# Kernel tuning notes

Measured on AMD Instinct MI355X. Metric: run time of the kernel, lower is better.

The kernel has to match this reference:

```python
import jax, jax.numpy as jnp
import numpy as np

B, S, T = 4096, 2048, 2  # batch of conversations, turns per conversation, num_tags


def setup_inputs() -> dict:
    key = jax.random.key(0)
    k1, k2, k3, k4, k5, k6 = jax.random.split(key, 6)
    emissions = jax.random.normal(k1, (B, S, T), dtype=jnp.float32)
    # learned transition matrices for DistanceCRF branch order:
    # [even2odd, I0, D_consecutive, D_nonconsecutive]
    trans_params = jax.random.normal(k2, (4, T, T), dtype=jnp.float32) * 0.1
    tags = jax.random.randint(k3, (B, S), 0, T)
    who2who = jax.random.randint(k4, (B, S), 0, 2)
    intime = jax.random.randint(k5, (B, S), 0, 3)
    distance = jax.random.randint(k6, (B, S), 0, 4)
    return {"emissions": emissions, "trans_params": trans_params, "tags": tags,
            "who2who": who2who, "intime": intime, "distance": distance}


def _select_trans(trans_params, who2who, intime, distance):
    """Per-step transition matrix selection (DistanceCRF logic).
    Returns [B, S, T, T]."""
    Tn = trans_params.shape[-1]
    # index 0 = zero 'padding' matrix (who2who == -1 case)
    bank = jnp.concatenate([jnp.zeros((1, Tn, Tn), trans_params.dtype), trans_params], axis=0)
    sel = jnp.where(who2who == -1, 0,
          jnp.where(who2who == 1, 1,          # even2odd
          jnp.where(intime == 0, 2,           # I0
          jnp.where(distance == 0, 3, 4))))   # D_consecutive / D_nonconsecutive
    return bank[sel]


def reference(emissions, trans_params, tags, who2who, intime, distance):
    Bn, Sn, Tn = emissions.shape
    trans = _select_trans(trans_params, who2who, intime, distance)  # [B,S,T,T]

    # ---- gold path score ----
    em_gold = jnp.take_along_axis(emissions, tags[..., None], axis=-1)[..., 0].sum(-1)  # [B]
    oh_prev = jax.nn.one_hot(tags[:, :-1], Tn, dtype=emissions.dtype)  # [B,S-1,T]
    oh_cur = jax.nn.one_hot(tags[:, 1:], Tn, dtype=emissions.dtype)
    tr_gold = jnp.einsum('bsij,bsi,bsj->b', trans[:, 1:], oh_prev, oh_cur)  # [B]
    gold_score = em_gold + tr_gold

    # ---- log partition via forward recursion (note: transition added at t=0 too,
    # matching the original implementation) ----
    def step(alpha, xs):
        em_t, tr_t = xs  # [B,T], [B,T,T]
        new_alpha = jax.nn.logsumexp(alpha[:, :, None] + em_t[:, None, :] + tr_t, axis=1)
        return new_alpha, None

    alpha0 = jnp.zeros((Bn, Tn), emissions.dtype)
    xs = (jnp.swapaxes(emissions, 0, 1), jnp.swapaxes(trans, 0, 1))  # [S,B,T], [S,B,T,T]
    alpha, _ = jax.lax.scan(step, alpha0, xs)
    total_score = jax.nn.logsumexp(alpha, axis=-1)  # [B]

    return jnp.stack([gold_score, total_score])  # [2, B]
```

## Files before the change

### kernel.cpp

```cpp
#include <hip/hip_runtime.h>
#include <math.h>

#define Bn 4096
#define Sn 2048
#define BLOCK 1024

__global__ __launch_bounds__(BLOCK) void crf_fused(
    const float* __restrict__ emissions,
    const float* __restrict__ trans_params,
    const int*   __restrict__ tags,
    const int*   __restrict__ who2who,
    const int*   __restrict__ intime,
    const int*   __restrict__ distance,
    float*       __restrict__ out)
{
    const int b    = blockIdx.x;
    const int t    = threadIdx.x;
    const int lane = t & 63;
    const int wave = t >> 6;
    const long base = (long)b * Sn;

    __shared__ __align__(16) float lbank[20];
    __shared__ __align__(16) float ebank[20];
    __shared__ float sred[16][8];

    float4 e  = ((const float4*)(emissions + base * 2))[t];
    int2   tg = ((const int2*)(tags     + base))[t];
    int2   wh = ((const int2*)(who2who  + base))[t];
    int2   it = ((const int2*)(intime   + base))[t];
    int2   ds = ((const int2*)(distance + base))[t];
    int ptag = 0;
    if (lane == 0 && t > 0) ptag = tags[base + 2 * t - 1];

    if (t < 20) {
        float v = (t < 4) ? 0.0f : trans_params[t - 4];
        lbank[t] = v;
        ebank[t] = __expf(v);
    }
    __syncthreads();

    int sel0 = (wh.x == -1) ? 0 : (wh.x == 1) ? 1
             : (it.x == 0) ? 2 : (ds.x == 0) ? 3 : 4;
    int sel1 = (wh.y == -1) ? 0 : (wh.y == 1) ? 1
             : (it.y == 0) ? 2 : (ds.y == 0) ? 3 : 4;
    float4 P0 = *(const float4*)(ebank + sel0 * 4);
    float4 P1 = *(const float4*)(ebank + sel1 * 4);
    float x00 = __expf(e.x), x01 = __expf(e.y);
    float x10 = __expf(e.z), x11 = __expf(e.w);

    float a00 = P0.x * x00, a01 = P0.y * x01;
    float a10 = P0.z * x00, a11 = P0.w * x01;
    float b00 = P1.x * x10, b01 = P1.y * x11;
    float b10 = P1.z * x10, b11 = P1.w * x11;
    float m00 = fmaf(a00, b00, a01 * b10);
    float m01 = fmaf(a00, b01, a01 * b11);
    float m10 = fmaf(a10, b00, a11 * b10);
    float m11 = fmaf(a10, b01, a11 * b11);

    float gold = (tg.x ? e.y : e.x) + (tg.y ? e.w : e.z);
    int pt0 = __shfl_up(tg.y, 1);
    if (lane == 0) pt0 = ptag;
    if (t > 0)
        gold += lbank[(sel0 << 2) + (pt0 << 1) + tg.x];
    gold += lbank[(sel1 << 2) + (tg.x << 1) + tg.y];

    float mx  = fmaxf(fmaxf(m00, m01), fmaxf(m10, m11));
    float inv = 1.0f / mx;
    float L   = __logf(mx);
    m00 *= inv; m01 *= inv; m10 *= inv; m11 *= inv;

    #pragma unroll
    for (int m = 1; m < 64; m <<= 1) {
        float o00 = __shfl_xor(m00, m);
        float o01 = __shfl_xor(m01, m);
        float o10 = __shfl_xor(m10, m);
        float o11 = __shfl_xor(m11, m);
        float oL  = __shfl_xor(L, m);
        float og  = __shfl_xor(gold, m);
        bool up = (lane & m) != 0;
        float p00 = up ? o00 : m00, p01 = up ? o01 : m01;
        float p10 = up ? o10 : m10, p11 = up ? o11 : m11;
        float q00 = up ? m00 : o00, q01 = up ? m01 : o01;
        float q10 = up ? m10 : o10, q11 = up ? m11 : o11;
        m00 = fmaf(p00, q00, p01 * q10);
        m01 = fmaf(p00, q01, p01 * q11);
        m10 = fmaf(p10, q00, p11 * q10);
        m11 = fmaf(p10, q01, p11 * q11);
        L += oL;
        gold += og;
    }

    if (lane == 0) {
        float mx2  = fmaxf(fmaxf(m00, m01), fmaxf(m10, m11));
        float inv2 = 1.0f / mx2;
        sred[wave][0] = m00 * inv2;
        sred[wave][1] = m01 * inv2;
        sred[wave][2] = m10 * inv2;
        sred[wave][3] = m11 * inv2;
        sred[wave][4] = L + __logf(mx2);
        sred[wave][5] = gold;
    }
    __syncthreads();

    if (wave == 0 && lane < 16) {
        float r00 = sred[lane][0], r01 = sred[lane][1];
        float r10 = sred[lane][2], r11 = sred[lane][3];
        float rL  = sred[lane][4], rg  = sred[lane][5];
        #pragma unroll
        for (int m = 1; m < 16; m <<= 1) {
            float o00 = __shfl_xor(r00, m);
            float o01 = __shfl_xor(r01, m);
            float o10 = __shfl_xor(r10, m);
            float o11 = __shfl_xor(r11, m);
            float oL  = __shfl_xor(rL, m);
            float og  = __shfl_xor(rg, m);
            bool up = (lane & m) != 0;
            float p00 = up ? o00 : r00, p01 = up ? o01 : r01;
            float p10 = up ? o10 : r10, p11 = up ? o11 : r11;
            float q00 = up ? r00 : o00, q01 = up ? r01 : o01;
            float q10 = up ? r10 : o10, q11 = up ? r11 : o11;
            r00 = fmaf(p00, q00, p01 * q10);
            r01 = fmaf(p00, q01, p01 * q11);
            r10 = fmaf(p10, q00, p11 * q10);
            r11 = fmaf(p10, q01, p11 * q11);
            rL += oL;
            rg += og;
        }
        if (lane == 0) {
            float tot = rL + __logf(r00 + r01 + r10 + r11);
            out[b]      = rg;
            out[Bn + b] = tot;
        }
    }
}

extern "C" void kernel_launch(void* const* d_in, const int* in_sizes, int n_in,
                              void* d_out, int out_size, void* d_ws, size_t ws_size,
                              hipStream_t stream) {
    const float* emissions    = (const float*)d_in[0];
    const float* trans_params = (const float*)d_in[1];
    const int*   tags         = (const int*)d_in[2];
    const int*   who2who      = (const int*)d_in[3];
    const int*   intime       = (const int*)d_in[4];
    const int*   distance     = (const int*)d_in[5];
    float* out = (float*)d_out;

    crf_fused<<<dim3(Bn), dim3(BLOCK), 0, stream>>>(
        emissions, trans_params, tags, who2who, intime, distance, out);
}
```

Baseline: 199.7 us.

## Assign one wavefront per sequence and loop over tiles with prefetch

Replaces the 1024-thread-per-sequence block with one 64-lane wave per sequence, processing 16 tiles of 128 steps in a loop. Each tile's 2x2 transfer matrices are scanned by butterfly and folded into a running product, which removes the shared-memory cross-wave reduction and block-wide barrier. The next tile's inputs are register-prefetched to overlap loads with compute. The tradeoff is that each wave now runs a serial chain of 16 butterfly reductions, which lengthens per-sequence latency.

```diff
diff --git a/kernel.cpp b/kernel.cpp
--- a/kernel.cpp
+++ b/kernel.cpp
@@ -3,9 +3,10 @@
 
 #define Bn 4096
 #define Sn 2048
-#define BLOCK 1024
+#define BLOCK 256
+#define NTILE 16
 
-__global__ __launch_bounds__(BLOCK) void crf_fused(
+__global__ __launch_bounds__(BLOCK, 4) void crf_wave(
     const float* __restrict__ emissions,
     const float* __restrict__ trans_params,
     const int*   __restrict__ tags,
@@ -14,123 +15,116 @@
     const int*   __restrict__ distance,
     float*       __restrict__ out)
 {
-    const int b    = blockIdx.x;
-    const int t    = threadIdx.x;
-    const int lane = t & 63;
-    const int wave = t >> 6;
-    const long base = (long)b * Sn;
+    const int lane = threadIdx.x & 63;
+    const int g    = blockIdx.x * 4 + (threadIdx.x >> 6);
+    const long base = (long)g * Sn;
 
     __shared__ __align__(16) float lbank[20];
     __shared__ __align__(16) float ebank[20];
-    __shared__ float sred[16][8];
-
-    float4 e  = ((const float4*)(emissions + base * 2))[t];
-    int2   tg = ((const int2*)(tags     + base))[t];
-    int2   wh = ((const int2*)(who2who  + base))[t];
-    int2   it = ((const int2*)(intime   + base))[t];
-    int2   ds = ((const int2*)(distance + base))[t];
-    int ptag = 0;
-    if (lane == 0 && t > 0) ptag = tags[base + 2 * t - 1];
-
-    if (t < 20) {
-        float v = (t < 4) ? 0.0f : trans_params[t - 4];
-        lbank[t] = v;
-        ebank[t] = __expf(v);
+    if (threadIdx.x < 20) {
+        float v = (threadIdx.x < 4) ? 0.0f : trans_params[threadIdx.x - 4];
+        lbank[threadIdx.x] = v;
+        ebank[threadIdx.x] = __expf(v);
     }
     __syncthreads();
 
-    int sel0 = (wh.x == -1) ? 0 : (wh.x == 1) ? 1
-             : (it.x == 0) ? 2 : (ds.x == 0) ? 3 : 4;
-    int sel1 = (wh.y == -1) ? 0 : (wh.y == 1) ? 1
-             : (it.y == 0) ? 2 : (ds.y == 0) ? 3 : 4;
-    float4 P0 = *(const float4*)(ebank + sel0 * 4);
-    float4 P1 = *(const float4*)(ebank + sel1 * 4);
-    float x00 = __expf(e.x), x01 = __expf(e.y);
-    float x10 = __expf(e.z), x11 = __expf(e.w);
+    const float4* ep = (const float4*)(emissions + base * 2);
+    const int2*   tp = (const int2*)(tags     + base);
+    const int2*   wp = (const int2*)(who2who  + base);
+    const int2*   ip = (const int2*)(intime   + base);
+    const int2*   dp = (const int2*)(distance + base);
 
-    float a00 = P0.x * x00, a01 = P0.y * x01;
-    float a10 = P0.z * x00, a11 = P0.w * x01;
-    float b00 = P1.x * x10, b01 = P1.y * x11;
-    float b10 = P1.z * x10, b11 = P1.w * x11;
-    float m00 = fmaf(a00, b00, a01 * b10);
-    float m01 = fmaf(a00, b01, a01 * b11);
-    float m10 = fmaf(a10, b00, a11 * b10);
-    float m11 = fmaf(a10, b01, a11 * b11);
+    float4 e  = ep[lane];
+    int2   tg = tp[lane], wh = wp[lane], it = ip[lane], ds = dp[lane];
 
-    float gold = (tg.x ? e.y : e.x) + (tg.y ? e.w : e.z);
-    int pt0 = __shfl_up(tg.y, 1);
-    if (lane == 0) pt0 = ptag;
-    if (t > 0)
-        gold += lbank[(sel0 << 2) + (pt0 << 1) + tg.x];
-    gold += lbank[(sel1 << 2) + (tg.x << 1) + tg.y];
+    float r00 = 1.f, r01 = 0.f, r10 = 0.f, r11 = 0.f;
+    float Luni  = 0.0f;
+    float Llane = 0.0f;
+    float gold  = 0.0f;
+    int carry_tag = 0;
 
-    float mx  = fmaxf(fmaxf(m00, m01), fmaxf(m10, m11));
-    float inv = 1.0f / mx;
-    float L   = __logf(mx);
-    m00 *= inv; m01 *= inv; m10 *= inv; m11 *= inv;
+    for (int i = 0; i < NTILE; ++i) {
+        float4 e_n; int2 tg_n, wh_n, it_n, ds_n;
+        if (i + 1 < NTILE) {
+            int o = (i + 1) * 64 + lane;
+            e_n = ep[o]; tg_n = tp[o]; wh_n = wp[o];
+            it_n = ip[o]; ds_n = dp[o];
+        }
+
+        int sel0 = (wh.x == -1) ? 0 : (wh.x == 1) ? 1
+                 : (it.x == 0) ? 2 : (ds.x == 0) ? 3 : 4;
+        int sel1 = (wh.y == -1) ? 0 : (wh.y == 1) ? 1
+                 : (it.y == 0) ? 2 : (ds.y == 0) ? 3 : 4;
+        float4 P0 = *(const float4*)(ebank + sel0 * 4);
+        float4 P1 = *(const float4*)(ebank + sel1 * 4);
+        float x00 = __expf(e.x), x01 = __expf(e.y);
+        float x10 = __expf(e.z), x11 = __expf(e.w);
+        float a00 = P0.x * x00, a01 = P0.y * x01;
+        float a10 = P0.z * x00, a11 = P0.w * x01;
+        float b00 = P1.x * x10, b01 = P1.y * x11;
+        float b10 = P1.z * x10, b11 = P1.w * x11;
+        float m00 = fmaf(a00, b00, a01 * b10);
+        float m01 = fmaf(a00, b01, a01 * b11);
+        float m10 = fmaf(a10, b00, a11 * b10);
+        float m11 = fmaf(a10, b01, a11 * b11);
+
+        gold += (tg.x ? e.y : e.x) + (tg.y ? e.w : e.z);
+        int pt0 = __shfl_up(tg.y, 1);
+        if (lane == 0) pt0 = carry_tag;
+        if (i > 0 || lane > 0)
+            gold += lbank[(sel0 << 2) + (pt0 << 1) + tg.x];
+        gold += lbank[(sel1 << 2) + (tg.x << 1) + tg.y];
+        carry_tag = __shfl(tg.y, 63);
+
+        float mx  = fmaxf(fmaxf(m00, m01), fmaxf(m10, m11));
+        float inv = 1.0f / mx;
+        Llane += __logf(mx);
+        m00 *= inv; m01 *= inv; m10 *= inv; m11 *= inv;
+
+        #pragma unroll
+        for (int m = 1; m < 64; m <<= 1) {
+            float o00 = __shfl_xor(m00, m);
+            float o01 = __shfl_xor(m01, m);
+            float o10 = __shfl_xor(m10, m);
+            float o11 = __shfl_xor(m11, m);
+            bool up = (lane & m) != 0;
+            float p00 = up ? o00 : m00, p01 = up ? o01 : m01;
+            float p10 = up ? o10 : m10, p11 = up ? o11 : m11;
+            float q00 = up ? m00 : o00, q01 = up ? m01 : o01;
+            float q10 = up ? m10 : o10, q11 = up ? m11 : o11;
+            m00 = fmaf(p00, q00, p01 * q10);
+            m01 = fmaf(p00, q01, p01 * q11);
+            m10 = fmaf(p10, q00, p11 * q10);
+            m11 = fmaf(p10, q01, p11 * q11);
+        }
+
+        if (i == 0) {
+            r00 = m00; r01 = m01; r10 = m10; r11 = m11;
+        } else {
+            float n00 = fmaf(r00, m00, r01 * m10);
+            float n01 = fmaf(r00, m01, r01 * m11);
+            float n10 = fmaf(r10, m00, r11 * m10);
+            float n11 = fmaf(r10, m01, r11 * m11);
+            r00 = n00; r01 = n01; r10 = n10; r11 = n11;
+        }
+        float mx2  = fmaxf(fmaxf(r00, r01), fmaxf(r10, r11));
+        float inv2 = 1.0f / mx2;
+        Luni += __logf(mx2);
+        r00 *= inv2; r01 *= inv2; r10 *= inv2; r11 *= inv2;
+
+        e = e_n; tg = tg_n; wh = wh_n; it = it_n; ds = ds_n;
+    }
 
     #pragma unroll
     for (int m = 1; m < 64; m <<= 1) {
-        float o00 = __shfl_xor(m00, m);
-        float o01 = __shfl_xor(m01, m);
-        float o10 = __shfl_xor(m10, m);
-        float o11 = __shfl_xor(m11, m);
-        float oL  = __shfl_xor(L, m);
-        float og  = __shfl_xor(gold, m);
-        bool up = (lane & m) != 0;
-        float p00 = up ? o00 : m00, p01 = up ? o01 : m01;
-        float p10 = up ? o10 : m10, p11 = up ? o11 : m11;
-        float q00 = up ? m00 : o00, q01 = up ? m01 : o01;
-        float q10 = up ? m10 : o10, q11 = up ? m11 : o11;
-        m00 = fmaf(p00, q00, p01 * q10);
-        m01 = fmaf(p00, q01, p01 * q11);
-        m10 = fmaf(p10, q00, p11 * q10);
-        m11 = fmaf(p10, q01, p11 * q11);
-        L += oL;
-        gold += og;
+        gold  += __shfl_xor(gold, m);
+        Llane += __shfl_xor(Llane, m);
     }
 
     if (lane == 0) {
-        float mx2  = fmaxf(fmaxf(m00, m01), fmaxf(m10, m11));
-        float inv2 = 1.0f / mx2;
-        sred[wave][0] = m00 * inv2;
-        sred[wave][1] = m01 * inv2;
-        sred[wave][2] = m10 * inv2;
-        sred[wave][3] = m11 * inv2;
-        sred[wave][4] = L + __logf(mx2);
-        sred[wave][5] = gold;
-    }
-    __syncthreads();
-
-    if (wave == 0 && lane < 16) {
-        float r00 = sred[lane][0], r01 = sred[lane][1];
-        float r10 = sred[lane][2], r11 = sred[lane][3];
-        float rL  = sred[lane][4], rg  = sred[lane][5];
-        #pragma unroll
-        for (int m = 1; m < 16; m <<= 1) {
-            float o00 = __shfl_xor(r00, m);
-            float o01 = __shfl_xor(r01, m);
-            float o10 = __shfl_xor(r10, m);
-            float o11 = __shfl_xor(r11, m);
-            float oL  = __shfl_xor(rL, m);
-            float og  = __shfl_xor(rg, m);
-            bool up = (lane & m) != 0;
-            float p00 = up ? o00 : r00, p01 = up ? o01 : r01;
-            float p10 = up ? o10 : r10, p11 = up ? o11 : r11;
-            float q00 = up ? r00 : o00, q01 = up ? r01 : o01;
-            float q10 = up ? r10 : o10, q11 = up ? r11 : o11;
-            r00 = fmaf(p00, q00, p01 * q10);
-            r01 = fmaf(p00, q01, p01 * q11);
-            r10 = fmaf(p10, q00, p11 * q10);
-            r11 = fmaf(p10, q01, p11 * q11);
-            rL += oL;
-            rg += og;
-        }
-        if (lane == 0) {
-            float tot = rL + __logf(r00 + r01 + r10 + r11);
-            out[b]      = rg;
-            out[Bn + b] = tot;
-        }
+        float tot = Luni + Llane + __logf(r00 + r01 + r10 + r11);
+        out[g]      = gold;
+        out[Bn + g] = tot;
     }
 }
 
@@ -145,6 +139,6 @@
     const int*   distance     = (const int*)d_in[5];
     float* out = (float*)d_out;
 
-    crf_fused<<<dim3(Bn), dim3(BLOCK), 0, stream>>>(
+    crf_wave<<<dim3(Bn / 4), dim3(BLOCK), 0, stream>>>(
         emissions, trans_params, tags, who2who, intime, distance, out);
 }
```

Result: slower. 207.6 us (+4.0%).

## Split CRF into stage kernel with 16-lane reduce and final cross-group reduce

Applied to the files above, without the earlier changes.

Replaces the single 1024-thread-per-batch kernel with two kernels. The first uses small 256-thread blocks, reduces 2x2 matrix products over 16-lane groups, and writes a per-group record to workspace with the normalized matrix packed as bf16. The second reduces the 64 groups per batch row in one wave. The aim is to drop the block-wide syncthreads and shared-memory reduction and improve occupancy for this bandwidth-bound load. The costs are an extra launch, a workspace round trip, bf16 precision loss on the intermediate products, and exp computed per element with the transition added instead of from a precomputed bank.

```diff
diff --git a/kernel.cpp b/kernel.cpp
--- a/kernel.cpp
+++ b/kernel.cpp
@@ -3,71 +3,116 @@
 
 #define Bn 4096
 #define Sn 2048
-#define BLOCK 1024
+#define NPAIR (Bn * (Sn / 2))
+#define K1B 256
+#define K1G (NPAIR / K1B)
+#define NGRP 64
 
-__global__ __launch_bounds__(BLOCK) void crf_fused(
+__device__ __forceinline__ unsigned pack_bf16(float x, float y) {
+    unsigned bx = __float_as_uint(x);
+    unsigned by = __float_as_uint(y);
+    bx += 0x7FFFu + ((bx >> 16) & 1);
+    by += 0x7FFFu + ((by >> 16) & 1);
+    return (bx >> 16) | (by & 0xFFFF0000u);
+}
+
+__global__ __launch_bounds__(K1B) void crf_stage(
     const float* __restrict__ emissions,
     const float* __restrict__ trans_params,
     const int*   __restrict__ tags,
     const int*   __restrict__ who2who,
     const int*   __restrict__ intime,
     const int*   __restrict__ distance,
-    float*       __restrict__ out)
+    float4*      __restrict__ ws)
 {
-    const int b    = blockIdx.x;
-    const int t    = threadIdx.x;
-    const int lane = t & 63;
-    const int wave = t >> 6;
-    const long base = (long)b * Sn;
+    const int t    = blockIdx.x * K1B + threadIdx.x;
+    const int lane = threadIdx.x & 63;
+    const int j    = t & 1023;
 
-    __shared__ __align__(16) float lbank[20];
-    __shared__ __align__(16) float ebank[20];
-    __shared__ float sred[16][8];
+    float4 e  = ((const float4*)emissions)[t];
+    int2   tg = ((const int2*)tags)[t];
+    int2   wh = ((const int2*)who2who)[t];
+    int2   i2 = ((const int2*)intime)[t];
+    int2   d2 = ((const int2*)distance)[t];
+    int ptag = 0;
+    if (lane == 0 && j != 0) ptag = tags[2 * t - 1];
 
-    float4 e  = ((const float4*)(emissions + base * 2))[t];
-    int2   tg = ((const int2*)(tags     + base))[t];
-    int2   wh = ((const int2*)(who2who  + base))[t];
-    int2   it = ((const int2*)(intime   + base))[t];
-    int2   ds = ((const int2*)(distance + base))[t];
-    int ptag = 0;
-    if (lane == 0 && t > 0) ptag = tags[base + 2 * t - 1];
+    int sel0 = (wh.x == -1) ? -1 : (wh.x == 1) ? 0
+             : (i2.x == 0) ? 1 : (d2.x == 0) ? 2 : 3;
+    int sel1 = (wh.y == -1) ? -1 : (wh.y == 1) ? 0
+             : (i2.y == 0) ? 1 : (d2.y == 0) ? 2 : 3;
+    float4 T0 = ((const float4*)trans_params)[sel0 < 0 ? 0 : sel0];
+    float4 T1 = ((const float4*)trans_params)[sel1 < 0 ? 0 : sel1];
+    if (sel0 < 0) T0 = make_float4(0.f, 0.f, 0.f, 0.f);
+    if (sel1 < 0) T1 = make_float4(0.f, 0.f, 0.f, 0.f);
 
-    if (t < 20) {
-        float v = (t < 4) ? 0.0f : trans_params[t - 4];
-        lbank[t] = v;
-        ebank[t] = __expf(v);
-    }
-    __syncthreads();
-
-    int sel0 = (wh.x == -1) ? 0 : (wh.x == 1) ? 1
-             : (it.x == 0) ? 2 : (ds.x == 0) ? 3 : 4;
-    int sel1 = (wh.y == -1) ? 0 : (wh.y == 1) ? 1
-             : (it.y == 0) ? 2 : (ds.y == 0) ? 3 : 4;
-    float4 P0 = *(const float4*)(ebank + sel0 * 4);
-    float4 P1 = *(const float4*)(ebank + sel1 * 4);
-    float x00 = __expf(e.x), x01 = __expf(e.y);
-    float x10 = __expf(e.z), x11 = __expf(e.w);
-
-    float a00 = P0.x * x00, a01 = P0.y * x01;
-    float a10 = P0.z * x00, a11 = P0.w * x01;
-    float b00 = P1.x * x10, b01 = P1.y * x11;
-    float b10 = P1.z * x10, b11 = P1.w * x11;
-    float m00 = fmaf(a00, b00, a01 * b10);
-    float m01 = fmaf(a00, b01, a01 * b11);
-    float m10 = fmaf(a10, b00, a11 * b10);
-    float m11 = fmaf(a10, b01, a11 * b11);
+    float a00 = __expf(T0.x + e.x), a01 = __expf(T0.y + e.y);
+    float a10 = __expf(T0.z + e.x), a11 = __expf(T0.w + e.y);
+    float c00 = __expf(T1.x + e.z), c01 = __expf(T1.y + e.w);
+    float c10 = __expf(T1.z + e.z), c11 = __expf(T1.w + e.w);
+    float m00 = fmaf(a00, c00, a01 * c10);
+    float m01 = fmaf(a00, c01, a01 * c11);
+    float m10 = fmaf(a10, c00, a11 * c10);
+    float m11 = fmaf(a10, c01, a11 * c11);
 
     float gold = (tg.x ? e.y : e.x) + (tg.y ? e.w : e.z);
     int pt0 = __shfl_up(tg.y, 1);
     if (lane == 0) pt0 = ptag;
-    if (t > 0)
-        gold += lbank[(sel0 << 2) + (pt0 << 1) + tg.x];
-    gold += lbank[(sel1 << 2) + (tg.x << 1) + tg.y];
+    if (j > 0)
+        gold += pt0 ? (tg.x ? T0.w : T0.z) : (tg.x ? T0.y : T0.x);
+    gold += tg.x ? (tg.y ? T1.w : T1.z) : (tg.y ? T1.y : T1.x);
 
     float mx  = fmaxf(fmaxf(m00, m01), fmaxf(m10, m11));
     float inv = 1.0f / mx;
     float L   = __logf(mx);
     m00 *= inv; m01 *= inv; m10 *= inv; m11 *= inv;
+
+    #pragma unroll
+    for (int m = 1; m < 16; m <<= 1) {
+        float o00 = __shfl_xor(m00, m);
+        float o01 = __shfl_xor(m01, m);
+        float o10 = __shfl_xor(m10, m);
+        float o11 = __shfl_xor(m11, m);
+        float oL  = __shfl_xor(L, m);
+        float og  = __shfl_xor(gold, m);
+        bool up = (lane & m) != 0;
+        float p00 = up ? o00 : m00, p01 = up ? o01 : m01;
+        float p10 = up ? o10 : m10, p11 = up ? o11 : m11;
+        float q00 = up ? m00 : o00, q01 = up ? m01 : o01;
+        float q10 = up ? m10 : o10, q11 = up ? m11 : o11;
+        m00 = fmaf(p00, q00, p01 * q10);
+        m01 = fmaf(p00, q01, p01 * q11);
+        m10 = fmaf(p10, q00, p11 * q10);
+        m11 = fmaf(p10, q01, p11 * q11);
+        L += oL;
+        gold += og;
+    }
+
+    if ((lane & 15) == 0) {
+        float mx2  = fmaxf(fmaxf(m00, m01), fmaxf(m10, m11));
+        float inv2 = 1.0f / mx2;
+        L += __logf(mx2);
+        unsigned u01 = pack_bf16(m00 * inv2, m01 * inv2);
+        unsigned u23 = pack_bf16(m10 * inv2, m11 * inv2);
+        ws[t >> 4] = make_float4(__uint_as_float(u01), __uint_as_float(u23),
+                                 L, gold);
+    }
+}
+
+__global__ __launch_bounds__(256) void crf_final(
+    const float4* __restrict__ ws,
+    float*        __restrict__ out)
+{
+    const int lane = threadIdx.x & 63;
+    const int b    = blockIdx.x * 4 + (threadIdx.x >> 6);
+
+    float4 r = ws[b * NGRP + lane];
+    unsigned u01 = __float_as_uint(r.x), u23 = __float_as_uint(r.y);
+    float m00 = __uint_as_float(u01 << 16);
+    float m01 = __uint_as_float(u01 & 0xFFFF0000u);
+    float m10 = __uint_as_float(u23 << 16);
+    float m11 = __uint_as_float(u23 & 0xFFFF0000u);
+    float L = r.z, gold = r.w;
 
     #pragma unroll
     for (int m = 1; m < 64; m <<= 1) {
@@ -91,46 +136,9 @@
     }
 
     if (lane == 0) {
-        float mx2  = fmaxf(fmaxf(m00, m01), fmaxf(m10, m11));
-        float inv2 = 1.0f / mx2;
-        sred[wave][0] = m00 * inv2;
-        sred[wave][1] = m01 * inv2;
-        sred[wave][2] = m10 * inv2;
-        sred[wave][3] = m11 * inv2;
-        sred[wave][4] = L + __logf(mx2);
-        sred[wave][5] = gold;
-    }
-    __syncthreads();
-
-    if (wave == 0 && lane < 16) {
-        float r00 = sred[lane][0], r01 = sred[lane][1];
-        float r10 = sred[lane][2], r11 = sred[lane][3];
-        float rL  = sred[lane][4], rg  = sred[lane][5];
-        #pragma unroll
-        for (int m = 1; m < 16; m <<= 1) {
-            float o00 = __shfl_xor(r00, m);
-            float o01 = __shfl_xor(r01, m);
-            float o10 = __shfl_xor(r10, m);
-            float o11 = __shfl_xor(r11, m);
-            float oL  = __shfl_xor(rL, m);
-            float og  = __shfl_xor(rg, m);
-            bool up = (lane & m) != 0;
-            float p00 = up ? o00 : r00, p01 = up ? o01 : r01;
-            float p10 = up ? o10 : r10, p11 = up ? o11 : r11;
-            float q00 = up ? r00 : o00, q01 = up ? r01 : o01;
-            float q10 = up ? r10 : o10, q11 = up ? r11 : o11;
-            r00 = fmaf(p00, q00, p01 * q10);
-            r01 = fmaf(p00, q01, p01 * q11);
-            r10 = fmaf(p10, q00, p11 * q10);
-            r11 = fmaf(p10, q01, p11 * q11);
-            rL += oL;
-            rg += og;
-        }
-        if (lane == 0) {
-            float tot = rL + __logf(r00 + r01 + r10 + r11);
-            out[b]      = rg;
-            out[Bn + b] = tot;
-        }
+        float tot = L + __logf(m00 + m01 + m10 + m11);
+        out[b]      = gold;
+        out[Bn + b] = tot;
     }
 }
 
@@ -144,7 +152,9 @@
     const int*   intime       = (const int*)d_in[4];
     const int*   distance     = (const int*)d_in[5];
     float* out = (float*)d_out;
+    float4* ws = (float4*)d_ws;
 
-    crf_fused<<<dim3(Bn), dim3(BLOCK), 0, stream>>>(
-        emissions, trans_params, tags, who2who, intime, distance, out);
+    crf_stage<<<dim3(K1G), dim3(K1B), 0, stream>>>(
+        emissions, trans_params, tags, who2who, intime, distance, ws);
+    crf_final<<<dim3(Bn / 4), dim3(256), 0, stream>>>(ws, out);
 }
```

Result: no change. 201.3 us (+0.8%).
